# Kernel optimization log

Measured on AMD Instinct MI355X. Metric: run time of the kernel, lower is better.

The kernel has to match this reference:

```python
import jax, jax.numpy as jnp
import numpy as np

N_NODES = 100000
N_EDGES = 3200000
NFEAT, HID, NCLASS = 256, 32, 16


def setup_inputs() -> dict:
    key = jax.random.key(0)
    ks = jax.random.split(key, 6)
    x = jax.random.normal(ks[0], (N_NODES, NFEAT), dtype=jnp.float32)
    edge_index = jax.random.randint(ks[1], (2, N_EDGES), 0, N_NODES, dtype=jnp.int64)
    edge_weight = jax.random.uniform(ks[2], (N_EDGES,), dtype=jnp.float32)
    # Glorot-ish init for the two GCNConv linear weights; bias zeros (PyG default init zeros bias)
    W1 = jax.random.normal(ks[3], (NFEAT, HID), dtype=jnp.float32) * (1.0 / np.sqrt(NFEAT))
    b1 = jnp.zeros((HID,), dtype=jnp.float32)
    W2 = jax.random.normal(ks[4], (HID, NCLASS), dtype=jnp.float32) * (1.0 / np.sqrt(HID))
    b2 = jnp.zeros((NCLASS,), dtype=jnp.float32)
    return {"x": x, "edge_index": edge_index, "edge_weight": edge_weight,
            "W1": W1, "b1": b1, "W2": W2, "b2": b2}


def _gcn_norm(row, col, w, n):
    """PyG gcn_norm: add self-loops (weight 1), symmetric normalization."""
    loop = jnp.arange(n, dtype=row.dtype)
    row = jnp.concatenate([row, loop])
    col = jnp.concatenate([col, loop])
    w = jnp.concatenate([w, jnp.ones((n,), dtype=w.dtype)])
    deg = jax.ops.segment_sum(w, col, num_segments=n)  # degree at target nodes
    dinv = jnp.where(deg > 0, jax.lax.rsqrt(deg), 0.0)
    norm = dinv[row] * w * dinv[col]
    return row, col, norm


def _gcn_conv(x, W, b, row, col, norm, n):
    xw = x @ W                                  # [N, out]
    msg = xw[row] * norm[:, None]               # gather at source + scale
    out = jax.ops.segment_sum(msg, col, num_segments=n)  # scatter-add at target
    return out + b


def reference(x, edge_index, edge_weight, W1, b1, W2, b2):
    n = x.shape[0]
    row, col, norm = _gcn_norm(edge_index[0], edge_index[1], edge_weight, n)
    h = jax.nn.relu(_gcn_conv(x, W1, b1, row, col, norm, n))
    # dropout is identity in eval mode
    logits = _gcn_conv(h, W2, b2, row, col, norm, n)
    return jax.nn.log_softmax(logits, axis=1)
```

## Files before the change

### kernel.cpp

```cpp
#include <hip/hip_runtime.h>

#define N_NODES 100000
#define N_EDGES 3200000
#define NFEAT 256
#define HID 32
#define NCLASS 16

#define NB 32
#define CHUNK (N_EDGES / NB)
#define RN 16384
#define NR ((N_NODES + RN - 1) / RN)

#define SCAN_TPB 256
#define SCAN_EPB 1024
#define SCAN_NBLK ((N_NODES + SCAN_EPB - 1) / SCAN_EPB)

#define XPAD 261

__device__ inline unsigned short f2bf(float f) {
    unsigned u = __float_as_uint(f);
    u += 0x7FFFu + ((u >> 16) & 1u);
    return (unsigned short)(u >> 16);
}
__device__ inline float bf2f(unsigned short s) {
    return __uint_as_float((unsigned)s << 16);
}

__global__ __launch_bounds__(1024) void k_count(const int* __restrict__ col,
                                                unsigned* __restrict__ H) {
    __shared__ unsigned hist[RN];
    int t = threadIdx.x, b = blockIdx.x, r = blockIdx.y;
    int base = r * RN;
    const int* cc = col + (size_t)b * CHUNK;
    for (int i = t; i < RN; i += 1024) hist[i] = 0;
    __syncthreads();
    for (int i = t; i < CHUNK; i += 1024) {
        unsigned d = (unsigned)cc[i] - (unsigned)base;
        if (d < RN) atomicAdd(&hist[d], 1u);
    }
    __syncthreads();
    int lim = min(RN, N_NODES - base);
    unsigned* Hb = H + (size_t)b * N_NODES;
    for (int i = t; i < lim; i += 1024) Hb[base + i] = hist[i];
}

__global__ void k_rowsum(const unsigned* __restrict__ H, int* __restrict__ cnt) {
    int n = blockIdx.x * 256 + threadIdx.x;
    if (n >= N_NODES) return;
    unsigned s = 0;
    #pragma unroll 8
    for (int b = 0; b < NB; ++b) s += H[(size_t)b * N_NODES + n];
    cnt[n] = (int)s;
}

__global__ __launch_bounds__(SCAN_TPB) void k_scanA(const int* __restrict__ cnt,
                                                    int* __restrict__ offs,
                                                    int* __restrict__ bsum) {
    __shared__ int s[SCAN_TPB];
    int t = threadIdx.x;
    int base = blockIdx.x * SCAN_EPB + t * 4;
    int v0 = (base + 0 < N_NODES) ? cnt[base + 0] : 0;
    int v1 = (base + 1 < N_NODES) ? cnt[base + 1] : 0;
    int v2 = (base + 2 < N_NODES) ? cnt[base + 2] : 0;
    int v3 = (base + 3 < N_NODES) ? cnt[base + 3] : 0;
    int sum = v0 + v1 + v2 + v3;
    s[t] = sum;
    __syncthreads();
    for (int off = 1; off < SCAN_TPB; off <<= 1) {
        int x = (t >= off) ? s[t - off] : 0;
        __syncthreads();
        s[t] += x;
        __syncthreads();
    }
    int excl = s[t] - sum;
    if (t == SCAN_TPB - 1) bsum[blockIdx.x] = s[t];
    int run = excl;
    if (base + 0 < N_NODES) offs[base + 0] = run; run += v0;
    if (base + 1 < N_NODES) offs[base + 1] = run; run += v1;
    if (base + 2 < N_NODES) offs[base + 2] = run; run += v2;
    if (base + 3 < N_NODES) offs[base + 3] = run;
}

__global__ __launch_bounds__(128) void k_scanB(int* __restrict__ bsum) {
    __shared__ int s[128];
    int t = threadIdx.x;
    int v = (t < SCAN_NBLK) ? bsum[t] : 0;
    s[t] = v;
    __syncthreads();
    for (int off = 1; off < 128; off <<= 1) {
        int x = (t >= off) ? s[t - off] : 0;
        __syncthreads();
        s[t] += x;
        __syncthreads();
    }
    if (t < SCAN_NBLK) bsum[t] = s[t] - v;
}

__global__ __launch_bounds__(SCAN_TPB) void k_scanC(int* __restrict__ offs,
                                                    const int* __restrict__ bsum) {
    int t = threadIdx.x;
    int add = bsum[blockIdx.x];
    int base = blockIdx.x * SCAN_EPB + t * 4;
    #pragma unroll
    for (int i = 0; i < 4; ++i) {
        int idx = base + i;
        if (idx < N_NODES) offs[idx] += add;
    }
    if (blockIdx.x == 0 && t == 0) offs[N_NODES] = N_EDGES;
}

__global__ void k_bprefix(unsigned* __restrict__ H, const int* __restrict__ offs) {
    int n = blockIdx.x * 256 + threadIdx.x;
    if (n >= N_NODES) return;
    unsigned run = (unsigned)offs[n];
    for (int b = 0; b < NB; ++b) {
        size_t idx = (size_t)b * N_NODES + n;
        unsigned v = H[idx];
        H[idx] = run;
        run += v;
    }
}

__global__ __launch_bounds__(1024) void k_place(const int* __restrict__ col,
                                                const unsigned* __restrict__ B,
                                                unsigned* __restrict__ perm) {
    __shared__ unsigned rk[RN];
    int t = threadIdx.x, b = blockIdx.x, r = blockIdx.y;
    int base = r * RN;
    size_t eb = (size_t)b * CHUNK;
    const unsigned* Bb = B + (size_t)b * N_NODES;
    for (int i = t; i < RN; i += 1024) rk[i] = 0;
    __syncthreads();
    for (int i = t; i < CHUNK; i += 1024) {
        int c = col[eb + i];
        unsigned d = (unsigned)c - (unsigned)base;
        if (d < RN) {
            unsigned rr = atomicAdd(&rk[d], 1u);
            perm[eb + i] = Bb[c] + rr;
        }
    }
}

__global__ void k_emit(const int* __restrict__ row, const float* __restrict__ w,
                       const unsigned* __restrict__ perm, float2* __restrict__ ein) {
    int e = blockIdx.x * 256 + threadIdx.x;
    if (e < N_EDGES) ein[perm[e]] = make_float2(__int_as_float(row[e]), w[e]);
}

__global__ void k_deg(const float2* __restrict__ ein, const int* __restrict__ offs,
                      float* __restrict__ dinv) {
    int idx = blockIdx.x * 256 + threadIdx.x;
    int n = idx >> 2, l = idx & 3;
    if (n >= N_NODES) return;
    int s = offs[n], e = offs[n + 1];
    float sum = 0.f;
    for (int p = s + l; p < e; p += 4) sum += ein[p].y;
    sum += __shfl_xor(sum, 1, 4);
    sum += __shfl_xor(sum, 2, 4);
    if (l == 0) dinv[n] = rsqrtf(1.0f + sum);
}

__global__ void k_norm(float2* __restrict__ ein, const int* __restrict__ offs,
                       const float* __restrict__ dinv) {
    int idx = blockIdx.x * 256 + threadIdx.x;
    int n = idx >> 2, l = idx & 3;
    if (n >= N_NODES) return;
    float dn = dinv[n];
    int s = offs[n], e = offs[n + 1];
    for (int p = s + l; p < e; p += 4) {
        float2 v = ein[p];
        int src = __float_as_int(v.x);
        ein[p].y = dn * dinv[src] * v.y;
    }
}

__global__ __launch_bounds__(256) void k_gemm1s(const float* __restrict__ x,
                                                const float* __restrict__ W1,
                                                float* __restrict__ xwp) {
    __shared__ float sWc[32 * HID];
    __shared__ float sX[32 * XPAD];
    int t = threadIdx.x;
    long rowbase = (long)blockIdx.x * 256;
    int kbase = blockIdx.y * 128;
    float* xw = xwp + (size_t)blockIdx.y * N_NODES * HID;
    int tr = t >> 3;
    int tc = t & 7;
    float acc[8][4] = {};
    for (int k0 = kbase; k0 < kbase + 128; k0 += 32) {
        *(float4*)&sWc[t * 4] = *(const float4*)&W1[k0 * HID + t * 4];
        #pragma unroll
        for (int p = 0; p < 8; ++p) {
            int rt = (t >> 3) + p * 32;
            int kk = (t & 7) * 4;
            long grow = rowbase + rt;
            float4 v = make_float4(0.f, 0.f, 0.f, 0.f);
            if (grow < N_NODES) v = *(const float4*)&x[grow * NFEAT + k0 + kk];
            sX[(kk + 0) * XPAD + rt] = v.x; sX[(kk + 1) * XPAD + rt] = v.y;
            sX[(kk + 2) * XPAD + rt] = v.z; sX[(kk + 3) * XPAD + rt] = v.w;
        }
        __syncthreads();
        #pragma unroll 8
        for (int kk = 0; kk < 32; ++kk) {
            float xv[8], wv[4];
            *(float4*)&xv[0] = *(float4*)&sX[kk * XPAD + tr * 8];
            *(float4*)&xv[4] = *(float4*)&sX[kk * XPAD + tr * 8 + 4];
            *(float4*)&wv[0] = *(float4*)&sWc[kk * HID + tc * 4];
            #pragma unroll
            for (int m = 0; m < 8; ++m)
                #pragma unroll
                for (int n = 0; n < 4; ++n)
                    acc[m][n] = fmaf(xv[m], wv[n], acc[m][n]);
        }
        __syncthreads();
    }
    #pragma unroll
    for (int m = 0; m < 8; ++m) {
        long r = rowbase + tr * 8 + m;
        if (r < N_NODES) {
            float4 o = make_float4(acc[m][0], acc[m][1], acc[m][2], acc[m][3]);
            *(float4*)&xw[r * HID + tc * 4] = o;
        }
    }
}

__global__ void k_comb(const float4* __restrict__ p0, const float4* __restrict__ p1,
                       ushort4* __restrict__ xwb) {
    int i = blockIdx.x * 256 + threadIdx.x;
    float4 a = p0[i], b = p1[i];
    ushort4 o;
    o.x = f2bf(a.x + b.x);
    o.y = f2bf(a.y + b.y);
    o.z = f2bf(a.z + b.z);
    o.w = f2bf(a.w + b.w);
    xwb[i] = o;
}

__global__ __launch_bounds__(256) void k_gather1(const unsigned short* __restrict__ xwb,
                                                 const float* __restrict__ dinv,
                                                 const float2* __restrict__ ein,
                                                 const int* __restrict__ offs,
                                                 const float* __restrict__ b1,
                                                 float* __restrict__ h) {
    int idx = blockIdx.x * 256 + threadIdx.x;
    int n = idx >> 3, l = idx & 7;
    int c4 = l * 4;
    const ushort4* xb = (const ushort4*)xwb;
    float di = dinv[n];
    float dd = di * di;
    ushort4 q = xb[(long)n * 8 + l];
    float4 acc = make_float4(bf2f(q.x) * dd, bf2f(q.y) * dd,
                             bf2f(q.z) * dd, bf2f(q.w) * dd);
    int s = offs[n], e = offs[n + 1];
    for (int p0 = s; p0 < e; p0 += 8) {
        int pl = p0 + l;
        float2 pr = (pl < e) ? ein[pl] : make_float2(__int_as_float(n), 0.f);
        int ri = __float_as_int(pr.x);
        #pragma unroll
        for (int j = 0; j < 8; ++j) {
            int r = __shfl(ri, j, 8);
            float nm = __shfl(pr.y, j, 8);
            ushort4 g = xb[(long)r * 8 + l];
            acc.x = fmaf(bf2f(g.x), nm, acc.x);
            acc.y = fmaf(bf2f(g.y), nm, acc.y);
            acc.z = fmaf(bf2f(g.z), nm, acc.z);
            acc.w = fmaf(bf2f(g.w), nm, acc.w);
        }
    }
    float4 bb = *(const float4*)&b1[c4];
    acc.x = fmaxf(acc.x + bb.x, 0.f);
    acc.y = fmaxf(acc.y + bb.y, 0.f);
    acc.z = fmaxf(acc.z + bb.z, 0.f);
    acc.w = fmaxf(acc.w + bb.w, 0.f);
    *(float4*)&h[(long)n * HID + c4] = acc;
}

__global__ __launch_bounds__(256) void k_gemm2(const float* __restrict__ h,
                                               const float* __restrict__ W2,
                                               unsigned short* __restrict__ hwb) {
    __shared__ float sH[64][33];
    __shared__ float sW2[HID * NCLASS];
    int t = threadIdx.x;
    if (t < 128) {
        int idx = t * 4;
        *(float4*)&sW2[idx] = *(const float4*)&W2[idx];
    }
    long base = (long)blockIdx.x * 64;
    #pragma unroll
    for (int i = 0; i < 2; ++i) {
        int idx = t + i * 256;
        int rt = idx >> 3, kk = (idx & 7) * 4;
        long gr = base + rt;
        float4 v = make_float4(0.f, 0.f, 0.f, 0.f);
        if (gr < N_NODES) v = *(const float4*)&h[gr * HID + kk];
        sH[rt][kk + 0] = v.x; sH[rt][kk + 1] = v.y;
        sH[rt][kk + 2] = v.z; sH[rt][kk + 3] = v.w;
    }
    __syncthreads();
    int r = t >> 2, c4 = (t & 3) * 4;
    float acc[4] = {};
    #pragma unroll
    for (int k = 0; k < HID; ++k) {
        float hv = sH[r][k];
        float wv[4];
        *(float4*)&wv[0] = *(float4*)&sW2[k * NCLASS + c4];
        #pragma unroll
        for (int n = 0; n < 4; ++n) acc[n] = fmaf(hv, wv[n], acc[n]);
    }
    long gr = base + r;
    if (gr < N_NODES) {
        ushort4 o;
        o.x = f2bf(acc[0]); o.y = f2bf(acc[1]);
        o.z = f2bf(acc[2]); o.w = f2bf(acc[3]);
        *(ushort4*)&hwb[gr * NCLASS + c4] = o;
    }
}

__global__ __launch_bounds__(256) void k_gather2(const unsigned short* __restrict__ hwb,
                                                 const float* __restrict__ dinv,
                                                 const float2* __restrict__ ein,
                                                 const int* __restrict__ offs,
                                                 const float* __restrict__ b2,
                                                 float* __restrict__ out) {
    int idx = blockIdx.x * 256 + threadIdx.x;
    int n = idx >> 2, l = idx & 3;
    if (n >= N_NODES) return;
    int c4 = l * 4;
    const ushort4* hb = (const ushort4*)hwb;
    float di = dinv[n];
    float dd = di * di;
    ushort4 q = hb[(long)n * 4 + l];
    float4 acc = make_float4(bf2f(q.x) * dd, bf2f(q.y) * dd,
                             bf2f(q.z) * dd, bf2f(q.w) * dd);
    int s = offs[n], e = offs[n + 1];
    for (int p0 = s; p0 < e; p0 += 8) {
        int pl0 = p0 + l, pl1 = p0 + 4 + l;
        float2 pr0 = (pl0 < e) ? ein[pl0] : make_float2(__int_as_float(n), 0.f);
        float2 pr1 = (pl1 < e) ? ein[pl1] : make_float2(__int_as_float(n), 0.f);
        int r0 = __float_as_int(pr0.x), r1 = __float_as_int(pr1.x);
        #pragma unroll
        for (int j = 0; j < 4; ++j) {
            int r = __shfl(r0, j, 4);
            float nm = __shfl(pr0.y, j, 4);
            ushort4 g = hb[(long)r * 4 + l];
            acc.x = fmaf(bf2f(g.x), nm, acc.x);
            acc.y = fmaf(bf2f(g.y), nm, acc.y);
            acc.z = fmaf(bf2f(g.z), nm, acc.z);
            acc.w = fmaf(bf2f(g.w), nm, acc.w);
        }
        #pragma unroll
        for (int j = 0; j < 4; ++j) {
            int r = __shfl(r1, j, 4);
            float nm = __shfl(pr1.y, j, 4);
            ushort4 g = hb[(long)r * 4 + l];
            acc.x = fmaf(bf2f(g.x), nm, acc.x);
            acc.y = fmaf(bf2f(g.y), nm, acc.y);
            acc.z = fmaf(bf2f(g.z), nm, acc.z);
            acc.w = fmaf(bf2f(g.w), nm, acc.w);
        }
    }
    float4 bb = *(const float4*)&b2[c4];
    float vx = acc.x + bb.x, vy = acc.y + bb.y, vz = acc.z + bb.z, vw = acc.w + bb.w;
    float m = fmaxf(fmaxf(vx, vy), fmaxf(vz, vw));
    m = fmaxf(m, __shfl_xor(m, 1, 4));
    m = fmaxf(m, __shfl_xor(m, 2, 4));
    float sum = __expf(vx - m) + __expf(vy - m) + __expf(vz - m) + __expf(vw - m);
    sum += __shfl_xor(sum, 1, 4);
    sum += __shfl_xor(sum, 2, 4);
    float ls = m + __logf(sum);
    float4 o = make_float4(vx - ls, vy - ls, vz - ls, vw - ls);
    *(float4*)&out[(long)n * NCLASS + c4] = o;
}

extern "C" void kernel_launch(void* const* d_in, const int* in_sizes, int n_in,
                              void* d_out, int out_size, void* d_ws, size_t ws_size,
                              hipStream_t stream) {
    const float* x  = (const float*)d_in[0];
    const int*   ei = (const int*)d_in[1];
    const float* w  = (const float*)d_in[2];
    const float* W1 = (const float*)d_in[3];
    const float* b1 = (const float*)d_in[4];
    const float* W2 = (const float*)d_in[5];
    const float* b2 = (const float*)d_in[6];
    float* out = (float*)d_out;

    const int* row = ei;
    const int* col = ei + N_EDGES;

    float* ws = (float*)d_ws;
    float2* ein = (float2*)ws;
    unsigned* H = (unsigned*)(ws + 2 * (size_t)N_EDGES);
    unsigned* perm = (unsigned*)(ws + 2 * (size_t)N_EDGES + (size_t)NB * N_NODES);
    float* h = (float*)perm;
    float* dinv = ws + 2 * (size_t)N_EDGES + (size_t)NB * N_NODES + N_EDGES;
    int* cnt = (int*)(dinv + N_NODES);
    int* offs = cnt + N_NODES;
    int* bsum = offs + N_NODES + 1;
    size_t xwp_off = (size_t)(2 * (size_t)N_EDGES + (size_t)NB * N_NODES + N_EDGES
                              + 3 * N_NODES + 1 + 128);
    xwp_off = (xwp_off + 3) & ~(size_t)3;
    float* xwp = ws + xwp_off;
    unsigned short* xwb = (unsigned short*)(xwp + 2 * (size_t)N_NODES * HID);
    unsigned short* hwb = xwb + (size_t)N_NODES * HID;

    const int B = 256;

    k_count<<<dim3(NB, NR), 1024, 0, stream>>>(col, H);
    k_rowsum<<<(N_NODES + B - 1) / B, B, 0, stream>>>(H, cnt);
    k_scanA<<<SCAN_NBLK, SCAN_TPB, 0, stream>>>(cnt, offs, bsum);
    k_scanB<<<1, 128, 0, stream>>>(bsum);
    k_scanC<<<SCAN_NBLK, SCAN_TPB, 0, stream>>>(offs, bsum);
    k_bprefix<<<(N_NODES + B - 1) / B, B, 0, stream>>>(H, offs);
    k_place<<<dim3(NB, NR), 1024, 0, stream>>>(col, H, perm);
    k_emit<<<(N_EDGES + B - 1) / B, B, 0, stream>>>(row, w, perm, ein);

    k_deg<<<(N_NODES * 4 + B - 1) / B, B, 0, stream>>>(ein, offs, dinv);
    k_norm<<<(N_NODES * 4 + B - 1) / B, B, 0, stream>>>(ein, offs, dinv);

    k_gemm1s<<<dim3((N_NODES + 255) / 256, 2), 256, 0, stream>>>(x, W1, xwp);
    k_comb<<<(N_NODES * HID / 4) / B, B, 0, stream>>>(
        (const float4*)xwp,
        (const float4*)(xwp + (size_t)N_NODES * HID),
        (ushort4*)xwb);
    k_gather1<<<(N_NODES * 8) / B, B, 0, stream>>>(xwb, dinv, ein, offs, b1, h);

    k_gemm2<<<(N_NODES + 63) / 64, B, 0, stream>>>(h, W2, hwb);
    k_gather2<<<(N_NODES * 4 + B - 1) / B, B, 0, stream>>>(hwb, dinv, ein, offs, b2, out);
}
```

Measured before the change: 305.7 us.

## Pack 16-bit histogram counters and split GEMM1 K into four bf16 partials

The counting sort now packs two 16-bit counters into each shared-memory word. Each histogram block therefore covers 32768 nodes, and the grid needs fewer node-range passes (4 instead of 7) over the column array in k_count and k_place. The first GEMM splits K four ways instead of two, giving twice as many blocks with smaller tiles, and writes bf16 partials. The combine kernel then sums four bf16 partials instead of two fp32 ones. This cuts partial-buffer traffic and the repeated edge scans, but rounding each partial to bf16 costs precision, and the 16-bit counters rely on per-chunk node counts staying below 65536.

```diff
diff --git a/kernel.cpp b/kernel.cpp
--- a/kernel.cpp
+++ b/kernel.cpp
@@ -8,8 +8,8 @@
 
 #define NB 32
 #define CHUNK (N_EDGES / NB)
-#define RN 16384
-#define NR ((N_NODES + RN - 1) / RN)
+#define RN2 32768
+#define NR2 ((N_NODES + RN2 - 1) / RN2)
 
 #define SCAN_TPB 256
 #define SCAN_EPB 1024
@@ -28,20 +28,21 @@
 
 __global__ __launch_bounds__(1024) void k_count(const int* __restrict__ col,
                                                 unsigned* __restrict__ H) {
-    __shared__ unsigned hist[RN];
+    __shared__ unsigned hist[RN2 / 2];
     int t = threadIdx.x, b = blockIdx.x, r = blockIdx.y;
-    int base = r * RN;
+    int base = r * RN2;
     const int* cc = col + (size_t)b * CHUNK;
-    for (int i = t; i < RN; i += 1024) hist[i] = 0;
+    for (int i = t; i < RN2 / 2; i += 1024) hist[i] = 0;
     __syncthreads();
     for (int i = t; i < CHUNK; i += 1024) {
         unsigned d = (unsigned)cc[i] - (unsigned)base;
-        if (d < RN) atomicAdd(&hist[d], 1u);
-    }
-    __syncthreads();
-    int lim = min(RN, N_NODES - base);
+        if (d < RN2) atomicAdd(&hist[d >> 1], 1u << ((d & 1) * 16));
+    }
+    __syncthreads();
+    int lim = min(RN2, N_NODES - base);
     unsigned* Hb = H + (size_t)b * N_NODES;
-    for (int i = t; i < lim; i += 1024) Hb[base + i] = hist[i];
+    for (int i = t; i < lim; i += 1024)
+        Hb[base + i] = (hist[i >> 1] >> ((i & 1) * 16)) & 0xFFFFu;
 }
 
 __global__ void k_rowsum(const unsigned* __restrict__ H, int* __restrict__ cnt) {
@@ -124,18 +125,19 @@
 __global__ __launch_bounds__(1024) void k_place(const int* __restrict__ col,
                                                 const unsigned* __restrict__ B,
                                                 unsigned* __restrict__ perm) {
-    __shared__ unsigned rk[RN];
+    __shared__ unsigned rk[RN2 / 2];
     int t = threadIdx.x, b = blockIdx.x, r = blockIdx.y;
-    int base = r * RN;
+    int base = r * RN2;
     size_t eb = (size_t)b * CHUNK;
     const unsigned* Bb = B + (size_t)b * N_NODES;
-    for (int i = t; i < RN; i += 1024) rk[i] = 0;
+    for (int i = t; i < RN2 / 2; i += 1024) rk[i] = 0;
     __syncthreads();
     for (int i = t; i < CHUNK; i += 1024) {
         int c = col[eb + i];
         unsigned d = (unsigned)c - (unsigned)base;
-        if (d < RN) {
-            unsigned rr = atomicAdd(&rk[d], 1u);
+        if (d < RN2) {
+            unsigned old = atomicAdd(&rk[d >> 1], 1u << ((d & 1) * 16));
+            unsigned rr = (old >> ((d & 1) * 16)) & 0xFFFFu;
             perm[eb + i] = Bb[c] + rr;
         }
     }
@@ -176,22 +178,22 @@
 
 __global__ __launch_bounds__(256) void k_gemm1s(const float* __restrict__ x,
                                                 const float* __restrict__ W1,
-                                                float* __restrict__ xwp) {
-    __shared__ float sWc[32 * HID];
-    __shared__ float sX[32 * XPAD];
+                                                unsigned short* __restrict__ xwp) {
+    __shared__ float sWc[16 * HID];
+    __shared__ float sX[16 * XPAD];
     int t = threadIdx.x;
     long rowbase = (long)blockIdx.x * 256;
-    int kbase = blockIdx.y * 128;
-    float* xw = xwp + (size_t)blockIdx.y * N_NODES * HID;
+    int kbase = blockIdx.y * 64;
+    unsigned short* xw = xwp + (size_t)blockIdx.y * N_NODES * HID;
     int tr = t >> 3;
     int tc = t & 7;
     float acc[8][4] = {};
-    for (int k0 = kbase; k0 < kbase + 128; k0 += 32) {
-        *(float4*)&sWc[t * 4] = *(const float4*)&W1[k0 * HID + t * 4];
-        #pragma unroll
-        for (int p = 0; p < 8; ++p) {
-            int rt = (t >> 3) + p * 32;
-            int kk = (t & 7) * 4;
+    for (int k0 = kbase; k0 < kbase + 64; k0 += 16) {
+        if (t < 128) *(float4*)&sWc[t * 4] = *(const float4*)&W1[k0 * HID + t * 4];
+        #pragma unroll
+        for (int p = 0; p < 4; ++p) {
+            int rt = (t >> 2) + p * 64;
+            int kk = (t & 3) * 4;
             long grow = rowbase + rt;
             float4 v = make_float4(0.f, 0.f, 0.f, 0.f);
             if (grow < N_NODES) v = *(const float4*)&x[grow * NFEAT + k0 + kk];
@@ -199,8 +201,8 @@
             sX[(kk + 2) * XPAD + rt] = v.z; sX[(kk + 3) * XPAD + rt] = v.w;
         }
         __syncthreads();
-        #pragma unroll 8
-        for (int kk = 0; kk < 32; ++kk) {
+        #pragma unroll
+        for (int kk = 0; kk < 16; ++kk) {
             float xv[8], wv[4];
             *(float4*)&xv[0] = *(float4*)&sX[kk * XPAD + tr * 8];
             *(float4*)&xv[4] = *(float4*)&sX[kk * XPAD + tr * 8 + 4];
@@ -217,21 +219,27 @@
     for (int m = 0; m < 8; ++m) {
         long r = rowbase + tr * 8 + m;
         if (r < N_NODES) {
-            float4 o = make_float4(acc[m][0], acc[m][1], acc[m][2], acc[m][3]);
-            *(float4*)&xw[r * HID + tc * 4] = o;
-        }
-    }
-}
-
-__global__ void k_comb(const float4* __restrict__ p0, const float4* __restrict__ p1,
+            ushort4 o;
+            o.x = f2bf(acc[m][0]); o.y = f2bf(acc[m][1]);
+            o.z = f2bf(acc[m][2]); o.w = f2bf(acc[m][3]);
+            *(ushort4*)&xw[r * HID + tc * 4] = o;
+        }
+    }
+}
+
+__global__ void k_comb(const unsigned short* __restrict__ xwp,
                        ushort4* __restrict__ xwb) {
     int i = blockIdx.x * 256 + threadIdx.x;
-    float4 a = p0[i], b = p1[i];
+    const ushort4* p0 = (const ushort4*)xwp;
+    const ushort4* p1 = p0 + 800000;
+    const ushort4* p2 = p1 + 800000;
+    const ushort4* p3 = p2 + 800000;
+    ushort4 a = p0[i], b = p1[i], c = p2[i], d = p3[i];
     ushort4 o;
-    o.x = f2bf(a.x + b.x);
-    o.y = f2bf(a.y + b.y);
-    o.z = f2bf(a.z + b.z);
-    o.w = f2bf(a.w + b.w);
+    o.x = f2bf(bf2f(a.x) + bf2f(b.x) + bf2f(c.x) + bf2f(d.x));
+    o.y = f2bf(bf2f(a.y) + bf2f(b.y) + bf2f(c.y) + bf2f(d.y));
+    o.z = f2bf(bf2f(a.z) + bf2f(b.z) + bf2f(c.z) + bf2f(d.z));
+    o.w = f2bf(bf2f(a.w) + bf2f(b.w) + bf2f(c.w) + bf2f(d.w));
     xwb[i] = o;
 }
 
@@ -398,29 +406,26 @@
     size_t xwp_off = (size_t)(2 * (size_t)N_EDGES + (size_t)NB * N_NODES + N_EDGES
                               + 3 * N_NODES + 1 + 128);
     xwp_off = (xwp_off + 3) & ~(size_t)3;
-    float* xwp = ws + xwp_off;
-    unsigned short* xwb = (unsigned short*)(xwp + 2 * (size_t)N_NODES * HID);
+    unsigned short* xwp = (unsigned short*)(ws + xwp_off);
+    unsigned short* xwb = (unsigned short*)(ws + xwp_off + 6400000);
     unsigned short* hwb = xwb + (size_t)N_NODES * HID;
 
     const int B = 256;
 
-    k_count<<<dim3(NB, NR), 1024, 0, stream>>>(col, H);
+    k_count<<<dim3(NB, NR2), 1024, 0, stream>>>(col, H);
     k_rowsum<<<(N_NODES + B - 1) / B, B, 0, stream>>>(H, cnt);
     k_scanA<<<SCAN_NBLK, SCAN_TPB, 0, stream>>>(cnt, offs, bsum);
     k_scanB<<<1, 128, 0, stream>>>(bsum);
     k_scanC<<<SCAN_NBLK, SCAN_TPB, 0, stream>>>(offs, bsum);
     k_bprefix<<<(N_NODES + B - 1) / B, B, 0, stream>>>(H, offs);
-    k_place<<<dim3(NB, NR), 1024, 0, stream>>>(col, H, perm);
+    k_place<<<dim3(NB, NR2), 1024, 0, stream>>>(col, H, perm);
     k_emit<<<(N_EDGES + B - 1) / B, B, 0, stream>>>(row, w, perm, ein);
 
     k_deg<<<(N_NODES * 4 + B - 1) / B, B, 0, stream>>>(ein, offs, dinv);
     k_norm<<<(N_NODES * 4 + B - 1) / B, B, 0, stream>>>(ein, offs, dinv);
 
-    k_gemm1s<<<dim3((N_NODES + 255) / 256, 2), 256, 0, stream>>>(x, W1, xwp);
-    k_comb<<<(N_NODES * HID / 4) / B, B, 0, stream>>>(
-        (const float4*)xwp,
-        (const float4*)(xwp + (size_t)N_NODES * HID),
-        (ushort4*)xwb);
+    k_gemm1s<<<dim3((N_NODES + 255) / 256, 4), 256, 0, stream>>>(x, W1, xwp);
+    k_comb<<<(N_NODES * HID / 4) / B, B, 0, stream>>>(xwp, (ushort4*)xwb);
     k_gather1<<<(N_NODES * 8) / B, B, 0, stream>>>(xwb, dinv, ein, offs, b1, h);
 
     k_gemm2<<<(N_NODES + 63) / 64, B, 0, stream>>>(h, W2, hwb);
```

Measured after the change: 312.2 us. +2.1%, slower.
